# Optimization experiments

Hardware: AMD Instinct MI355X
Metric: run time of the kernel (lower is better)

The kernel has to match this reference:

```python
import jax, jax.numpy as jnp
import numpy as np

D_MODEL = 512
B, T = 2, 4096
LN_EPS = 1e-5


def _layernorm(x, gamma, beta):
    mu = jnp.mean(x, axis=-1, keepdims=True)
    var = jnp.mean((x - mu) ** 2, axis=-1, keepdims=True)
    return (x - mu) * jax.lax.rsqrt(var + LN_EPS) * gamma + beta


def setup_inputs() -> dict:
    key = jax.random.key(0)
    ks = jax.random.split(key, 16)
    d = D_MODEL
    s = 1.0 / np.sqrt(d)
    inp = {
        "tokens": jax.random.normal(ks[0], (B, T, d), dtype=jnp.float32),
        "Wq": jax.random.normal(ks[1], (d, d), dtype=jnp.float32) * s,
        "bq": jnp.zeros((d,), jnp.float32),
        "Wk": jax.random.normal(ks[2], (d, d), dtype=jnp.float32) * s,
        "bk": jnp.zeros((d,), jnp.float32),
        "Wv": jax.random.normal(ks[3], (d, d), dtype=jnp.float32) * s,
        "bv": jnp.zeros((d,), jnp.float32),
        "distance_scale": jnp.asarray(0.01, jnp.float32),
        "W1": jax.random.normal(ks[4], (d, 4 * d), dtype=jnp.float32) * s,
        "b1": jnp.zeros((4 * d,), jnp.float32),
        "W2": jax.random.normal(ks[5], (4 * d, d), dtype=jnp.float32) * (1.0 / np.sqrt(4 * d)),
        "b2": jnp.zeros((d,), jnp.float32),
        "g1": jnp.ones((d,), jnp.float32),
        "be1": jnp.zeros((d,), jnp.float32),
        "g2": jnp.ones((d,), jnp.float32),
        "be2": jnp.zeros((d,), jnp.float32),
    }
    return inp


def reference(tokens, Wq, bq, Wk, bk, Wv, bv, distance_scale,
              W1, b1, W2, b2, g1, be1, g2, be2):
    Bv, Tv, d = tokens.shape
    q = tokens @ Wq + bq
    k = tokens @ Wk + bk
    v = tokens @ Wv + bv
    # [B, T, T] raw scores
    scores = jnp.einsum('btd,bsd->bts', q, k)
    pos = jnp.arange(Tv)
    distance = jnp.abs(pos[None, :] - pos[:, None]).astype(jnp.float32)  # [T, T]
    scores = scores + (-distance_scale * distance)[None, :, :]
    causal = pos[None, :] > pos[:, None]  # strict upper triangle
    scores = jnp.where(causal[None, :, :], -jnp.inf, scores)
    scores = scores / jnp.sqrt(jnp.asarray(d, jnp.float32))
    attn = jax.nn.softmax(scores, axis=-1)
    attn_out = jnp.einsum('bts,bsd->btd', attn, v)
    x = _layernorm(tokens + attn_out, g1, be1)
    y = jnp.maximum(x @ W1 + b1, 0.0) @ W2 + b2
    z = _layernorm(y + x, g2, be2)
    return z
```

## Files before the change

kernel.cpp:

```cpp
#include <hip/hip_runtime.h>
#include <hip/hip_bf16.h>
#include <math.h>

typedef unsigned short u16;
typedef __attribute__((ext_vector_type(8))) short short8;
typedef __attribute__((ext_vector_type(4))) float float4v;

#define MFMA_BF16(a, b, c) __builtin_amdgcn_mfma_f32_16x16x32_bf16((a), (b), (c), 0, 0, 0)

typedef const __attribute__((address_space(1))) void* gas_ptr;
typedef __attribute__((address_space(3))) void* las_ptr;

__device__ __forceinline__ u16 f2bf(float f) {
  __hip_bfloat16 h = __float2bfloat16(f);
  return __builtin_bit_cast(u16, h);
}

__device__ __forceinline__ float bf2f(u16 v) {
  return __builtin_bit_cast(float, (unsigned)v << 16);
}

__device__ __forceinline__ void load_lds16(const u16* g, u16* l) {
  __builtin_amdgcn_global_load_lds((gas_ptr)g, (las_ptr)l, 16, 0, 0);
}

__device__ __forceinline__ int xcd_swz(int bid, int nwg) {
  return (bid & 7) * (nwg >> 3) + (bid >> 3);
}

__device__ __forceinline__ void gemm_mainloop_sb(
    const u16* __restrict__ A, const u16* __restrict__ Bt,
    int kb, int kend, int lda, int ldb,
    int m0, int n0, u16* As, u16* Bs, float4v acc[4][4])
{
  const int tid = threadIdx.x;
  const int w = tid >> 6, lane = tid & 63;
  const int wr = w >> 1, wc = w & 1;
  const int lr = lane & 15, lk = (lane >> 4) * 8;
  for (int k0 = kb; k0 < kend; k0 += 32) {
#pragma unroll
    for (int c = 0; c < 2; ++c) {
      int idx = c * 256 + w * 64 + lane;
      int r = idx >> 2, c8 = idx & 3;
      load_lds16(A + (size_t)(m0 + r) * lda + k0 + c8 * 8, As + (size_t)(c * 256 + w * 64) * 8);
      load_lds16(Bt + (size_t)(n0 + r) * ldb + k0 + c8 * 8, Bs + (size_t)(c * 256 + w * 64) * 8);
    }
    __syncthreads();
    short8 af[4], bf[4];
#pragma unroll
    for (int mt = 0; mt < 4; ++mt)
      af[mt] = *(const short8*)&As[(wr * 64 + mt * 16 + lr) * 32 + lk];
#pragma unroll
    for (int nt = 0; nt < 4; ++nt)
      bf[nt] = *(const short8*)&Bs[(wc * 64 + nt * 16 + lr) * 32 + lk];
#pragma unroll
    for (int mt = 0; mt < 4; ++mt)
#pragma unroll
      for (int nt = 0; nt < 4; ++nt)
        acc[mt][nt] = MFMA_BF16(af[mt], bf[nt], acc[mt][nt]);
    __syncthreads();
  }
}

__device__ __forceinline__ void gemm_mainloop_p3(
    const u16* __restrict__ A, const u16* __restrict__ Bt,
    int kb, int kend, int lda, int ldb,
    int m0, int n0, u16* As, u16* Bs, float4v acc[4][4])
{
  const int tid = threadIdx.x;
  const int w = tid >> 6, lane = tid & 63;
  const int wr = w >> 1, wc = w & 1;
  const int lr = lane & 15, lk = (lane >> 4) * 8;

  auto stage = [&](int buf, int k0) {
#pragma unroll
    for (int c = 0; c < 2; ++c) {
      int idx = c * 256 + w * 64 + lane;
      int r = idx >> 2, c8 = idx & 3;
      load_lds16(A + (size_t)(m0 + r) * lda + k0 + c8 * 8,
                 As + buf * 4096 + (size_t)(c * 256 + w * 64) * 8);
      load_lds16(Bt + (size_t)(n0 + r) * ldb + k0 + c8 * 8,
                 Bs + buf * 4096 + (size_t)(c * 256 + w * 64) * 8);
    }
  };

  const int nt = (kend - kb) >> 5;
  stage(0, kb);
  if (nt > 1) stage(1, kb + 32);
  if (nt > 2) stage(2, kb + 64);
  int buf = 0;
  for (int t = 0; t < nt; ++t) {
    const int ahead = nt - 1 - t;
    if (ahead >= 2)      asm volatile("s_waitcnt vmcnt(8)\n\ts_barrier" ::: "memory");
    else if (ahead == 1) asm volatile("s_waitcnt vmcnt(4)\n\ts_barrier" ::: "memory");
    else                 asm volatile("s_waitcnt vmcnt(0)\n\ts_barrier" ::: "memory");
    const u16* Ab = As + buf * 4096;
    const u16* Bb = Bs + buf * 4096;
    short8 af[4], bf[4];
#pragma unroll
    for (int mt = 0; mt < 4; ++mt)
      af[mt] = *(const short8*)&Ab[(wr * 64 + mt * 16 + lr) * 32 + lk];
#pragma unroll
    for (int nt2 = 0; nt2 < 4; ++nt2)
      bf[nt2] = *(const short8*)&Bb[(wc * 64 + nt2 * 16 + lr) * 32 + lk];
#pragma unroll
    for (int mt = 0; mt < 4; ++mt)
#pragma unroll
      for (int nt2 = 0; nt2 < 4; ++nt2)
        acc[mt][nt2] = MFMA_BF16(af[mt], bf[nt2], acc[mt][nt2]);
    if (t + 3 < nt) {
      asm volatile("s_waitcnt lgkmcnt(0)\n\ts_barrier" ::: "memory");
      stage(buf, kb + (t + 3) * 32);
    }
    buf = (buf == 2) ? 0 : buf + 1;
  }
}

__global__ __launch_bounds__(256) void gemm_qkv(
    const u16* __restrict__ A, const u16* __restrict__ Bt,
    const float* __restrict__ bq, const float* __restrict__ bk, const float* __restrict__ bv,
    u16* __restrict__ qo, u16* __restrict__ ko, u16* __restrict__ vo)
{
  __shared__ u16 As[3 * 128 * 32], Bs[3 * 128 * 32];
  float4v acc[4][4];
#pragma unroll
  for (int mt = 0; mt < 4; ++mt)
#pragma unroll
    for (int nt = 0; nt < 4; ++nt) acc[mt][nt] = (float4v){0.f, 0.f, 0.f, 0.f};
  const int s = xcd_swz(blockIdx.x + 12 * blockIdx.y, 12 * 64);
  const int m0 = (s / 12) * 128, n0 = (s % 12) * 128;
  gemm_mainloop_p3(A, Bt, 0, 512, 512, 512, m0, n0, As, Bs, acc);
  const int tid = threadIdx.x, w = tid >> 6, lane = tid & 63;
  const int wr = w >> 1, wc = w & 1, lr = lane & 15, lg = lane >> 4;
#pragma unroll
  for (int mt = 0; mt < 4; ++mt) {
#pragma unroll
    for (int nt = 0; nt < 4; ++nt) {
      int n = n0 + wc * 64 + nt * 16 + lr;
#pragma unroll
      for (int r = 0; r < 4; ++r) {
        int i = m0 + wr * 64 + mt * 16 + lg * 4 + r;
        float v = acc[mt][nt][r];
        if (n < 512) {
          qo[(size_t)i * 512 + n] = f2bf(v + bq[n]);
        } else if (n < 1024) {
          ko[(size_t)i * 512 + (n - 512)] = f2bf(v + bk[n - 512]);
        } else {
          vo[(size_t)i * 512 + (n - 1024)] = f2bf(v + bv[n - 1024]);
        }
      }
    }
  }
}

__global__ __launch_bounds__(256) void transpose_v_kernel(
    const u16* __restrict__ src, u16* __restrict__ dst)
{
  __shared__ u16 tile[32][33];
  const int b = blockIdx.z;
  const int t0 = blockIdx.x * 32, d0 = blockIdx.y * 32;
  const u16* sp = src + (size_t)b * 4096 * 512;
  u16* dp = dst + (size_t)b * 512 * 4096;
  const int tx = threadIdx.x & 31, ty = threadIdx.x >> 5;
#pragma unroll
  for (int i = 0; i < 32; i += 8)
    tile[ty + i][tx] = sp[(size_t)(t0 + ty + i) * 512 + d0 + tx];
  __syncthreads();
#pragma unroll
  for (int i = 0; i < 32; i += 8)
    dp[(size_t)(d0 + ty + i) * 4096 + t0 + tx] = tile[tx][ty + i];
}

__global__ __launch_bounds__(256) void gemm_qk_p(
    const u16* __restrict__ q, const u16* __restrict__ k,
    const float* __restrict__ dsp,
    u16* __restrict__ P, float* __restrict__ l)
{
  __shared__ u16 As[128 * 32], Bs[128 * 32];
  float4v acc[4][4];
#pragma unroll
  for (int mt = 0; mt < 4; ++mt)
#pragma unroll
    for (int nt = 0; nt < 4; ++nt) acc[mt][nt] = (float4v){0.f, 0.f, 0.f, 0.f};
  const int b = blockIdx.y;
  const u16* qb = q + (size_t)b * 4096 * 512;
  const u16* kb = k + (size_t)b * 4096 * 512;
  u16* Pb = P + (size_t)b * 4096 * 4096;
  float* lb = l + b * 4096;
  int idx = blockIdx.x;
  int tm = (int)((sqrtf(8.0f * (float)idx + 1.0f) - 1.0f) * 0.5f);
  while ((tm + 1) * (tm + 2) / 2 <= idx) ++tm;
  while (tm * (tm + 1) / 2 > idx) --tm;
  int tn = idx - tm * (tm + 1) / 2;
  const int m0 = tm * 128, n0 = tn * 128;
  gemm_mainloop_sb(qb, kb, 0, 512, 512, 512, m0, n0, As, Bs, acc);
  const int tid = threadIdx.x, w = tid >> 6, lane = tid & 63;
  const int wr = w >> 1, wc = w & 1, lr = lane & 15, lg = lane >> 4;
  const float invs = 0.04419417382415922f;
  const float dsi = dsp[0] * invs;
  const float L2E = 1.4426950408889634f;
  float rs[4][4];
#pragma unroll
  for (int mt = 0; mt < 4; ++mt)
#pragma unroll
    for (int r = 0; r < 4; ++r) rs[mt][r] = 0.f;
#pragma unroll
  for (int mt = 0; mt < 4; ++mt) {
#pragma unroll
    for (int nt = 0; nt < 4; ++nt) {
      int j = n0 + wc * 64 + nt * 16 + lr;
#pragma unroll
      for (int r = 0; r < 4; ++r) {
        int i = m0 + wr * 64 + mt * 16 + lg * 4 + r;
        float x = acc[mt][nt][r] * invs - dsi * fabsf((float)(i - j));
        float p = (j > i) ? 0.f : exp2f(x * L2E);
        Pb[(size_t)i * 4096 + j] = f2bf(p);
        rs[mt][r] += p;
      }
    }
  }
#pragma unroll
  for (int mt = 0; mt < 4; ++mt) {
#pragma unroll
    for (int r = 0; r < 4; ++r) {
      float v = rs[mt][r];
#pragma unroll
      for (int off = 1; off < 16; off <<= 1) v += __shfl_xor(v, off, 64);
      if (lr == 0)
        atomicAdd(&lb[m0 + wr * 64 + mt * 16 + lg * 4 + r], v);
    }
  }
}

__global__ __launch_bounds__(256) void gemm_pv(
    const u16* __restrict__ P, const u16* __restrict__ vt,
    float* __restrict__ y0, u16* __restrict__ y1,
    u16* __restrict__ y2, u16* __restrict__ y3)
{
  __shared__ u16 As[3 * 128 * 32], Bs[3 * 128 * 32];
  float4v acc[4][4];
#pragma unroll
  for (int mt = 0; mt < 4; ++mt)
#pragma unroll
    for (int nt = 0; nt < 4; ++nt) acc[mt][nt] = (float4v){0.f, 0.f, 0.f, 0.f};
  const int s = xcd_swz(blockIdx.x + 4 * (blockIdx.y + 80 * blockIdx.z), 640);
  const int b = s / 320;
  const int t2 = s % 320;
  const int xb = t2 % 4;
  int rem = t2 / 4;
  const u16* Pb = P + (size_t)b * 4096 * 4096;
  const u16* vb = vt + (size_t)b * 512 * 4096;
  int tm = 0, cpt = 1;
  while (rem >= cpt) { rem -= cpt; ++tm; cpt = (tm >> 3) + 1; }
  const int m0 = tm * 128, n0 = xb * 128;
  const int kb = rem * 1024;
  const int kfull = (tm + 1) * 128;
  const int kend = (kb + 1024 < kfull) ? (kb + 1024) : kfull;
  gemm_mainloop_p3(Pb, vb, kb, kend, 4096, 4096, m0, n0, As, Bs, acc);
  const int tid = threadIdx.x, w = tid >> 6, lane = tid & 63;
  const int wr = w >> 1, wc = w & 1, lr = lane & 15, lg = lane >> 4;
  const size_t bofs = (size_t)b * 4096 * 512;
#pragma unroll
  for (int mt = 0; mt < 4; ++mt) {
#pragma unroll
    for (int nt = 0; nt < 4; ++nt) {
      int n = n0 + wc * 64 + nt * 16 + lr;
#pragma unroll
      for (int r = 0; r < 4; ++r) {
        int i = m0 + wr * 64 + mt * 16 + lg * 4 + r;
        size_t o = bofs + (size_t)i * 512 + n;
        float v = acc[mt][nt][r];
        if (rem == 0)      y0[o] = v;
        else if (rem == 1) y1[o] = f2bf(v);
        else if (rem == 2) y2[o] = f2bf(v);
        else               y3[o] = f2bf(v);
      }
    }
  }
}

__global__ __launch_bounds__(256) void gemm_ffn1(
    const u16* __restrict__ A, const u16* __restrict__ Bt,
    const float* __restrict__ b1, u16* __restrict__ h)
{
  __shared__ u16 As[3 * 128 * 32], Bs[3 * 128 * 32];
  float4v acc[4][4];
#pragma unroll
  for (int mt = 0; mt < 4; ++mt)
#pragma unroll
    for (int nt = 0; nt < 4; ++nt) acc[mt][nt] = (float4v){0.f, 0.f, 0.f, 0.f};
  const int s = xcd_swz(blockIdx.x + 16 * blockIdx.y, 16 * 64);
  const int m0 = (s / 16) * 128, n0 = (s % 16) * 128;
  gemm_mainloop_p3(A, Bt, 0, 512, 512, 512, m0, n0, As, Bs, acc);
  const int tid = threadIdx.x, w = tid >> 6, lane = tid & 63;
  const int wr = w >> 1, wc = w & 1, lr = lane & 15, lg = lane >> 4;
#pragma unroll
  for (int mt = 0; mt < 4; ++mt) {
#pragma unroll
    for (int nt = 0; nt < 4; ++nt) {
      int n = n0 + wc * 64 + nt * 16 + lr;
#pragma unroll
      for (int r = 0; r < 4; ++r) {
        int i = m0 + wr * 64 + mt * 16 + lg * 4 + r;
        h[(size_t)i * 2048 + n] = f2bf(fmaxf(acc[mt][nt][r] + b1[n], 0.f));
      }
    }
  }
}

__global__ __launch_bounds__(256) void gemm_ffn2(
    const u16* __restrict__ A, const u16* __restrict__ Bt,
    float* __restrict__ f0, u16* __restrict__ f1)
{
  __shared__ u16 As[3 * 128 * 32], Bs[3 * 128 * 32];
  float4v acc[4][4];
#pragma unroll
  for (int mt = 0; mt < 4; ++mt)
#pragma unroll
    for (int nt = 0; nt < 4; ++nt) acc[mt][nt] = (float4v){0.f, 0.f, 0.f, 0.f};
  const int s = xcd_swz(blockIdx.x + 4 * (blockIdx.y + 64 * blockIdx.z), 512);
  const int zz = s / 256;
  const int t2 = s % 256;
  const int m0 = (t2 / 4) * 128, n0 = (t2 % 4) * 128;
  const int kb = zz * 1024;
  gemm_mainloop_p3(A, Bt, kb, kb + 1024, 2048, 2048, m0, n0, As, Bs, acc);
  const int tid = threadIdx.x, w = tid >> 6, lane = tid & 63;
  const int wr = w >> 1, wc = w & 1, lr = lane & 15, lg = lane >> 4;
#pragma unroll
  for (int mt = 0; mt < 4; ++mt) {
#pragma unroll
    for (int nt = 0; nt < 4; ++nt) {
      int n = n0 + wc * 64 + nt * 16 + lr;
#pragma unroll
      for (int r = 0; r < 4; ++r) {
        int i = m0 + wr * 64 + mt * 16 + lg * 4 + r;
        if (zz == 0) f0[(size_t)i * 512 + n] = acc[mt][nt][r];
        else         f1[(size_t)i * 512 + n] = f2bf(acc[mt][nt][r]);
      }
    }
  }
}

__global__ __launch_bounds__(256) void ln1_kernel(
    const float* __restrict__ y0, const u16* __restrict__ y1,
    const u16* __restrict__ y2, const u16* __restrict__ y3,
    const float* __restrict__ lsum, const float* __restrict__ tok,
    const float* __restrict__ g, const float* __restrict__ be,
    float* __restrict__ of, u16* __restrict__ ob)
{
  const int row = blockIdx.x * 4 + (threadIdx.x >> 6);
  const int lane = threadIdx.x & 63;
  const int rloc = row & 4095;
  const size_t base = (size_t)row * 512 + lane * 8;
  const float linv = 1.0f / lsum[row];
  float v[8];
#pragma unroll
  for (int t = 0; t < 8; ++t) v[t] = y0[base + t];
  if (rloc >= 1024) {
#pragma unroll
    for (int t = 0; t < 8; ++t) v[t] += bf2f(y1[base + t]);
  }
  if (rloc >= 2048) {
#pragma unroll
    for (int t = 0; t < 8; ++t) v[t] += bf2f(y2[base + t]);
  }
  if (rloc >= 3072) {
#pragma unroll
    for (int t = 0; t < 8; ++t) v[t] += bf2f(y3[base + t]);
  }
#pragma unroll
  for (int t = 0; t < 8; ++t) v[t] = v[t] * linv + tok[base + t];
  float s = 0.f;
#pragma unroll
  for (int t = 0; t < 8; ++t) s += v[t];
#pragma unroll
  for (int off = 1; off < 64; off <<= 1) s += __shfl_xor(s, off, 64);
  const float mu = s * (1.0f / 512.0f);
  float qv = 0.f;
#pragma unroll
  for (int t = 0; t < 8; ++t) { float d = v[t] - mu; qv += d * d; }
#pragma unroll
  for (int off = 1; off < 64; off <<= 1) qv += __shfl_xor(qv, off, 64);
  const float rs = rsqrtf(qv * (1.0f / 512.0f) + 1e-5f);
  const int cb = lane * 8;
#pragma unroll
  for (int t = 0; t < 8; ++t) {
    float xv = (v[t] - mu) * rs * g[cb + t] + be[cb + t];
    of[base + t] = xv;
    ob[base + t] = f2bf(xv);
  }
}

__global__ __launch_bounds__(256) void ln2_kernel(
    const float* __restrict__ f0, const u16* __restrict__ f1,
    const float* __restrict__ b2, const float* __restrict__ bsrc,
    const float* __restrict__ g, const float* __restrict__ be,
    float* __restrict__ of)
{
  const int row = blockIdx.x * 4 + (threadIdx.x >> 6);
  const int lane = threadIdx.x & 63;
  const size_t base = (size_t)row * 512 + lane * 8;
  const int cb = lane * 8;
  float v[8];
#pragma unroll
  for (int t = 0; t < 8; ++t)
    v[t] = f0[base + t] + bf2f(f1[base + t]) + b2[cb + t] + bsrc[base + t];
  float s = 0.f;
#pragma unroll
  for (int t = 0; t < 8; ++t) s += v[t];
#pragma unroll
  for (int off = 1; off < 64; off <<= 1) s += __shfl_xor(s, off, 64);
  const float mu = s * (1.0f / 512.0f);
  float qv = 0.f;
#pragma unroll
  for (int t = 0; t < 8; ++t) { float d = v[t] - mu; qv += d * d; }
#pragma unroll
  for (int off = 1; off < 64; off <<= 1) qv += __shfl_xor(qv, off, 64);
  const float rs = rsqrtf(qv * (1.0f / 512.0f) + 1e-5f);
#pragma unroll
  for (int t = 0; t < 8; ++t) {
    float xv = (v[t] - mu) * rs * g[cb + t] + be[cb + t];
    of[base + t] = xv;
  }
}

__global__ __launch_bounds__(256) void cast_bf_kernel(
    const float* __restrict__ in, u16* __restrict__ out)
{
  const size_t i = ((size_t)blockIdx.x * 256 + threadIdx.x) * 8;
#pragma unroll
  for (int t = 0; t < 8; ++t) out[i + t] = f2bf(in[i + t]);
}

__global__ __launch_bounds__(256) void transpose_qkv_kernel(
    const float* __restrict__ Wq, const float* __restrict__ Wk,
    const float* __restrict__ Wv, u16* __restrict__ dst)
{
  __shared__ u16 tile[32][33];
  const float* src = (blockIdx.z == 0) ? Wq : (blockIdx.z == 1) ? Wk : Wv;
  u16* d = dst + (size_t)blockIdx.z * 512 * 512;
  const int tx = threadIdx.x & 31, ty = threadIdx.x >> 5;
  const int n0 = blockIdx.x * 32, k0 = blockIdx.y * 32;
#pragma unroll
  for (int i = 0; i < 32; i += 8)
    tile[ty + i][tx] = f2bf(src[(size_t)(k0 + ty + i) * 512 + n0 + tx]);
  __syncthreads();
#pragma unroll
  for (int i = 0; i < 32; i += 8)
    d[(size_t)(n0 + ty + i) * 512 + k0 + tx] = tile[tx][ty + i];
}

__global__ __launch_bounds__(256) void transpose_bf_kernel(
    const float* __restrict__ src, u16* __restrict__ dst, int K, int N)
{
  __shared__ u16 tile[32][33];
  const int tx = threadIdx.x & 31, ty = threadIdx.x >> 5;
  const int n0 = blockIdx.x * 32, k0 = blockIdx.y * 32;
#pragma unroll
  for (int i = 0; i < 32; i += 8)
    tile[ty + i][tx] = f2bf(src[(size_t)(k0 + ty + i) * N + n0 + tx]);
  __syncthreads();
#pragma unroll
  for (int i = 0; i < 32; i += 8)
    dst[(size_t)(n0 + ty + i) * K + k0 + tx] = tile[tx][ty + i];
}

extern "C" void kernel_launch(void* const* d_in, const int* in_sizes, int n_in,
                              void* d_out, int out_size, void* d_ws, size_t ws_size,
                              hipStream_t stream) {
  const float* tokens = (const float*)d_in[0];
  const float* Wq = (const float*)d_in[1];
  const float* bq = (const float*)d_in[2];
  const float* Wk = (const float*)d_in[3];
  const float* bk = (const float*)d_in[4];
  const float* Wv = (const float*)d_in[5];
  const float* bv = (const float*)d_in[6];
  const float* dscale = (const float*)d_in[7];
  const float* W1 = (const float*)d_in[8];
  const float* b1 = (const float*)d_in[9];
  const float* W2 = (const float*)d_in[10];
  const float* b2 = (const float*)d_in[11];
  const float* g1 = (const float*)d_in[12];
  const float* be1 = (const float*)d_in[13];
  const float* g2 = (const float*)d_in[14];
  const float* be2 = (const float*)d_in[15];
  float* out = (float*)d_out;

  char* ws = (char*)d_ws;
  u16*   tok_bf = (u16*)(ws + 0);
  u16*   wqkvT  = (u16*)(ws + 8388608);
  u16*   w1T    = (u16*)(ws + 9961472);
  u16*   w2T    = (u16*)(ws + 12058624);
  u16*   qbuf   = (u16*)(ws + 14155776);
  u16*   kbuf   = (u16*)(ws + 22544384);
  u16*   vtbuf  = (u16*)(ws + 30932992);
  u16*   Pbuf   = (u16*)(ws + 39321600);
  float* y0buf  = (float*)(ws + 106430464);
  u16*   y1buf  = (u16*)(ws + 123207680);
  u16*   y2buf  = (u16*)(ws + 131596288);
  u16*   y3buf  = (u16*)(ws + 139984896);
  float* xf     = (float*)(ws + 148373504);
  u16*   xbf    = (u16*)(ws + 165150720);
  u16*   hbuf   = (u16*)(ws + 173539328);
  float* f0buf  = (float*)(ws + 207093760);
  u16*   f1buf  = (u16*)(ws + 223870976);
  float* lbuf   = (float*)(ws + 232259584);
  u16*   vbuf   = (u16*)(ws + 232292352);

  (void)hipMemsetAsync(lbuf, 0, 2 * 4096 * sizeof(float), stream);

  cast_bf_kernel<<<2048, 256, 0, stream>>>(tokens, tok_bf);
  transpose_qkv_kernel<<<dim3(16, 16, 3), 256, 0, stream>>>(Wq, Wk, Wv, wqkvT);
  transpose_bf_kernel<<<dim3(64, 16), 256, 0, stream>>>(W1, w1T, 512, 2048);
  transpose_bf_kernel<<<dim3(16, 64), 256, 0, stream>>>(W2, w2T, 2048, 512);

  gemm_qkv<<<dim3(12, 64), 256, 0, stream>>>(tok_bf, wqkvT, bq, bk, bv, qbuf, kbuf, vbuf);
  transpose_v_kernel<<<dim3(128, 16, 2), 256, 0, stream>>>(vbuf, vtbuf);

  gemm_qk_p<<<dim3(528, 2), 256, 0, stream>>>(qbuf, kbuf, dscale, Pbuf, lbuf);
  gemm_pv<<<dim3(4, 80, 2), 256, 0, stream>>>(Pbuf, vtbuf, y0buf, y1buf, y2buf, y3buf);

  ln1_kernel<<<2048, 256, 0, stream>>>(y0buf, y1buf, y2buf, y3buf, lbuf, tokens,
                                       g1, be1, xf, xbf);

  gemm_ffn1<<<dim3(16, 64), 256, 0, stream>>>(xbf, w1T, b1, hbuf);

  gemm_ffn2<<<dim3(4, 64, 2), 256, 0, stream>>>(hbuf, w2T, f0buf, f1buf);

  ln2_kernel<<<2048, 256, 0, stream>>>(f0buf, f1buf, b2, xf, g2, be2, out);
}
```

Baseline: 298.4 us.

## Retile FFN1 GEMM to 256x256 blocks with 512 threads and BK=64 double buffer

Replaces the 128x128 tile FFN1 GEMM (1024 blocks, 3-stage BK=32 pipeline) with 256x256 tiles computed by 8 waves, each owning a 128x64 sub-tile. It uses a double-buffered BK=64 LDS pipeline with 128 KB dynamic shared memory and direct global-to-LDS loads. The aim is more operand reuse per LDS byte and fewer global loads of A and B. In exchange it runs only 256 blocks, so occupancy and wave-level overlap drop. It also uses a large LDS footprint and a 2-stage pipeline with raw waitcnt/barrier asm.

```diff
diff --git a/kernel.cpp b/kernel.cpp
--- a/kernel.cpp
+++ b/kernel.cpp
@@ -279,30 +279,76 @@
   }
 }
 
-__global__ __launch_bounds__(256) void gemm_ffn1(
+__global__ __launch_bounds__(512, 2) void gemm_ffn1(
     const u16* __restrict__ A, const u16* __restrict__ Bt,
     const float* __restrict__ b1, u16* __restrict__ h)
 {
-  __shared__ u16 As[3 * 128 * 32], Bs[3 * 128 * 32];
-  float4v acc[4][4];
-#pragma unroll
-  for (int mt = 0; mt < 4; ++mt)
+  extern __shared__ u16 lds[];
+  float4v acc[8][4];
+#pragma unroll
+  for (int mt = 0; mt < 8; ++mt)
 #pragma unroll
     for (int nt = 0; nt < 4; ++nt) acc[mt][nt] = (float4v){0.f, 0.f, 0.f, 0.f};
-  const int s = xcd_swz(blockIdx.x + 16 * blockIdx.y, 16 * 64);
-  const int m0 = (s / 16) * 128, n0 = (s % 16) * 128;
-  gemm_mainloop_p3(A, Bt, 0, 512, 512, 512, m0, n0, As, Bs, acc);
-  const int tid = threadIdx.x, w = tid >> 6, lane = tid & 63;
-  const int wr = w >> 1, wc = w & 1, lr = lane & 15, lg = lane >> 4;
-#pragma unroll
-  for (int mt = 0; mt < 4; ++mt) {
-#pragma unroll
-    for (int nt = 0; nt < 4; ++nt) {
-      int n = n0 + wc * 64 + nt * 16 + lr;
+  const int s = xcd_swz(blockIdx.x, 256);
+  const int m0 = (s >> 3) * 256, n0 = (s & 7) * 256;
+  const int tid = threadIdx.x;
+  const int w = tid >> 6, lane = tid & 63;
+  const int wr = w >> 2, wc = w & 3;
+  const int lr = lane & 15, lk = (lane >> 4) * 8;
+  const int r4 = lane >> 2, c4 = (lane & 3) * 8;
+
+  auto stage = [&](int buf, int k0) {
+#pragma unroll
+    for (int c = 0; c < 4; ++c) {
+      int ri = w + c * 8;
+      int p = ri >> 4, rg = ri & 15;
+      int row = rg * 16 + r4;
+      int col = p * 32 + c4;
+      u16* dA = lds + buf * 16384 + p * 8192 + rg * 512;
+      u16* dB = lds + 32768 + buf * 16384 + p * 8192 + rg * 512;
+      load_lds16(A + (size_t)(m0 + row) * 512 + k0 + col, dA);
+      load_lds16(Bt + (size_t)(n0 + row) * 512 + k0 + col, dB);
+    }
+  };
+
+  stage(0, 0);
+  stage(1, 64);
+  const int nt = 8;
+  for (int t = 0; t < nt; ++t) {
+    if (t < nt - 1) asm volatile("s_waitcnt vmcnt(8)\n\ts_barrier" ::: "memory");
+    else            asm volatile("s_waitcnt vmcnt(0)\n\ts_barrier" ::: "memory");
+    const u16* Ab = lds + (t & 1) * 16384;
+    const u16* Bb = lds + 32768 + (t & 1) * 16384;
+#pragma unroll
+    for (int ks = 0; ks < 2; ++ks) {
+      short8 af[8], bfr[4];
+#pragma unroll
+      for (int mt = 0; mt < 8; ++mt)
+        af[mt] = *(const short8*)&Ab[ks * 8192 + (wr * 128 + mt * 16 + lr) * 32 + lk];
+#pragma unroll
+      for (int nt2 = 0; nt2 < 4; ++nt2)
+        bfr[nt2] = *(const short8*)&Bb[ks * 8192 + (wc * 64 + nt2 * 16 + lr) * 32 + lk];
+#pragma unroll
+      for (int mt = 0; mt < 8; ++mt)
+#pragma unroll
+        for (int nt2 = 0; nt2 < 4; ++nt2)
+          acc[mt][nt2] = MFMA_BF16(af[mt], bfr[nt2], acc[mt][nt2]);
+    }
+    if (t + 2 < nt) {
+      asm volatile("s_waitcnt lgkmcnt(0)\n\ts_barrier" ::: "memory");
+      stage(t & 1, (t + 2) * 64);
+    }
+  }
+  const int lg = lane >> 4;
+#pragma unroll
+  for (int mt = 0; mt < 8; ++mt) {
+#pragma unroll
+    for (int nt2 = 0; nt2 < 4; ++nt2) {
+      int n = n0 + wc * 64 + nt2 * 16 + lr;
 #pragma unroll
       for (int r = 0; r < 4; ++r) {
-        int i = m0 + wr * 64 + mt * 16 + lg * 4 + r;
-        h[(size_t)i * 2048 + n] = f2bf(fmaxf(acc[mt][nt][r] + b1[n], 0.f));
+        int i = m0 + wr * 128 + mt * 16 + lg * 4 + r;
+        h[(size_t)i * 2048 + n] = f2bf(fmaxf(acc[mt][nt2][r] + b1[n], 0.f));
       }
     }
   }
@@ -523,7 +569,7 @@
   ln1_kernel<<<2048, 256, 0, stream>>>(y0buf, y1buf, y2buf, y3buf, lbuf, tokens,
                                        g1, be1, xf, xbf);
 
-  gemm_ffn1<<<dim3(16, 64), 256, 0, stream>>>(xbf, w1T, b1, hbuf);
+  gemm_ffn1<<<256, 512, 131072, stream>>>(xbf, w1T, b1, hbuf);
 
   gemm_ffn2<<<dim3(4, 64, 2), 256, 0, stream>>>(hbuf, w2T, f0buf, f1buf);
 
```

Measured after the change: 329.7 us. +10.5%, slower.
